# Optimization experiments

Hardware: AMD Instinct MI355X
Metric: run time of the kernel (lower is better)

The kernel has to match this reference:

```python
import math
import numpy as np
import jax, jax.numpy as jnp

# ---- e3nn-convention real Wigner 3j (small l, computed once in float64) ----

def _cg(j1, m1, j2, m2, j3, m3):
    if m3 != m1 + m2:
        return 0.0
    f = math.factorial
    vmin = max(-j1 + j2 + m3, -j1 + m1, 0)
    vmax = min(j2 + j3 + m1, j3 - j1 + j2, j3 + m3)
    c = math.sqrt((2 * j3 + 1) * f(j3 + j1 - j2) * f(j3 - j1 + j2) * f(j1 + j2 - j3)
                  * f(j3 + m3) * f(j3 - m3)
                  / (f(j1 + j2 + j3 + 1) * f(j1 - m1) * f(j1 + m1) * f(j2 - m2) * f(j2 + m2)))
    s = 0.0
    for v in range(vmin, vmax + 1):
        s += (-1.0) ** (v + j2 + m2) * f(j2 + j3 + m1 - v) * f(j1 - m1 + v) \
             / (f(v) * f(j3 - j1 + j2 - v) * f(j3 + m3 - v) * f(v + j1 - j2 - m3))
    return c * s


def _q(l):
    # real -> complex spherical-harmonic change of basis (e3nn convention)
    q = np.zeros((2 * l + 1, 2 * l + 1), dtype=np.complex128)
    for m in range(-l, 0):
        q[l + m, l + abs(m)] = 1.0 / math.sqrt(2)
        q[l + m, l - abs(m)] = -1j / math.sqrt(2)
    q[l, l] = 1.0
    for m in range(1, l + 1):
        q[l + m, l + abs(m)] = (-1) ** m / math.sqrt(2)
        q[l + m, l - abs(m)] = 1j * (-1) ** m / math.sqrt(2)
    return (-1j) ** l * q


def wigner_3j(l1, l2, l3):
    C = np.zeros((2 * l1 + 1, 2 * l2 + 1, 2 * l3 + 1))
    for m1 in range(-l1, l1 + 1):
        for m2 in range(-l2, l2 + 1):
            m3 = m1 + m2
            if -l3 <= m3 <= l3:
                C[m1 + l1, m2 + l2, m3 + l3] = _cg(l1, m1, l2, m2, l3, m3)
    Cr = np.einsum('ia,kb,mc,ikm->abc', _q(l1), _q(l2), np.conj(_q(l3)), C.astype(np.complex128))
    assert np.abs(Cr.imag).max() < 1e-8
    Cr = Cr.real
    return Cr / np.linalg.norm(Cr)  # unit Frobenius norm (e3nn wigner_3j)

W3J_101 = wigner_3j(1, 0, 1)  # (3,1,3)
W3J_121 = wigner_3j(1, 2, 1)  # (3,5,3)
W3J_221 = wigner_3j(2, 2, 1)  # (5,5,3)
W3J_321 = wigner_3j(3, 2, 1)  # (7,5,3)
W3J_110 = wigner_3j(1, 1, 0)
W3J_112 = wigner_3j(1, 1, 2)
# CartesianTensor('ij=ji') change of basis: symmetric 3x3 -> irreps 1x0e+1x2e, orthonormal rows
COB = np.concatenate([W3J_110[:, :, 0][None], math.sqrt(5.0) * np.moveaxis(W3J_112, 2, 0)], axis=0)  # (6,3,3)
# e3nn FullyConnectedTensorProduct path norm: irrep_normalization='component' (alpha=dim_out=3),
# path_normalization='element' (4 paths to same output, each mul1*mul2=2 elements -> x=8)
ALPHA = math.sqrt(3.0 / 8.0)
IDX = np.array([0, 4, 8, 1, 5, 6])  # xx,yy,zz,xy,yz,zx picks from flattened 3x3 jacobian

BS = 1_000_000


def setup_inputs():
    key = jax.random.key(0)
    node_feature = jax.random.normal(key, (BS, 64), dtype=jnp.float32)
    constant_w = jnp.ones((8,), dtype=jnp.float32)
    return {"node_feature": node_feature, "constant_w": constant_w}


def _piezo(node_feature, constant_w):
    bs = node_feature.shape[0]
    dt = node_feature.dtype
    # input irrep layout: 2x0e[0:2] 2x0o[2:4] 2x1e[4:10] 2x1o[10:16] 2x2e[16:26] 2x2o[26:36] 2x3e[36:50] 2x3o[50:64]
    x1o = node_feature[:, 10:16].reshape(bs, 2, 3)
    x2o = node_feature[:, 26:36].reshape(bs, 2, 5)
    x3o = node_feature[:, 50:64].reshape(bs, 2, 7)
    w = constant_w
    # D is bilinear in (node_feature, stress) and stress is linear in outer_S, so the three
    # autograd.grad calls in the original module exactly extract the (b,3,3,3) jacobian
    # dD/d(outer_S). Compute it analytically in one fused pass.
    # K[b,k,a] = dD[b,k]/dstress[b,a], stress irreps 1x0e(+)1x2e
    k0 = ALPHA * jnp.einsum('u,bui,ijk->bkj', w[0:2], x1o, jnp.asarray(W3J_101, dt))  # (b,3,1) from 0e
    k1 = ALPHA * jnp.einsum('u,bui,ijk->bkj', w[2:4], x1o, jnp.asarray(W3J_121, dt))  # (b,3,5) from 2e
    k2 = ALPHA * jnp.einsum('u,bui,ijk->bkj', w[4:6], x2o, jnp.asarray(W3J_221, dt))
    k3 = ALPHA * jnp.einsum('u,bui,ijk->bkj', w[6:8], x3o, jnp.asarray(W3J_321, dt))
    K = jnp.concatenate([k0, k1 + k2 + k3], axis=-1)  # (b,3,6)
    # chain rule through from_cartesian: stress[b,a] = sum_pq COB[a,p,q] * outer_S[b,p,q]
    J = jnp.einsum('bka,apq->bkpq', K, jnp.asarray(COB, dt)).reshape(bs, 3, 9)
    return J[:, :, IDX]  # (b, 3, 6)


def reference(node_feature, constant_w):
    return _piezo(node_feature, constant_w)
```

## Files before the change

### kernel.cpp

```cpp
#include <hip/hip_runtime.h>
#include <cmath>
#include <complex>
#include <algorithm>

#define TILE 256

struct PiezoConsts {
  float M1[3][3][6];
  float M2[3][3][6];
  float M3[5][3][6];
  float M4[7][3][6];
};

typedef std::complex<double> cd;

static double factd(int n) {
  static const double f[11] = {1,1,2,6,24,120,720,5040,40320,362880,3628800};
  return f[n];
}

static double cg_(int j1,int m1,int j2,int m2,int j3,int m3) {
  if (m3 != m1 + m2) return 0.0;
  int vmin = std::max(std::max(-j1 + j2 + m3, -j1 + m1), 0);
  int vmax = std::min(std::min(j2 + j3 + m1, j3 - j1 + j2), j3 + m3);
  double c = std::sqrt((2*j3+1) * factd(j3+j1-j2) * factd(j3-j1+j2) * factd(j1+j2-j3)
                       * factd(j3+m3) * factd(j3-m3)
                       / (factd(j1+j2+j3+1) * factd(j1-m1) * factd(j1+m1)
                          * factd(j2-m2) * factd(j2+m2)));
  double s = 0.0;
  for (int v = vmin; v <= vmax; ++v) {
    double sgn = ((v + j2 + m2) & 1) ? -1.0 : 1.0;
    s += sgn * factd(j2+j3+m1-v) * factd(j1-m1+v)
         / (factd(v) * factd(j3-j1+j2-v) * factd(j3+m3-v) * factd(v+j1-j2-m3));
  }
  return c * s;
}

static void q_mat(int l, cd q[7][7]) {
  for (int a=0;a<7;a++) for (int b=0;b<7;b++) q[a][b] = cd(0,0);
  double s2 = 1.0/std::sqrt(2.0);
  for (int m=-l; m<0; ++m) {
    q[l+m][l-m] = cd(s2, 0);
    q[l+m][l+m] = cd(0, -s2);
  }
  q[l][l] = cd(1,0);
  for (int m=1; m<=l; ++m) {
    double sg = (m & 1) ? -1.0 : 1.0;
    q[l+m][l+m] = cd(sg*s2, 0);
    q[l+m][l-m] = cd(0, sg*s2);
  }
  cd ph(1,0); const cd mi(0,-1);
  for (int t=0;t<l;t++) ph *= mi;
  int n = 2*l+1;
  for (int a=0;a<n;a++) for (int b=0;b<n;b++) q[a][b] *= ph;
}

static void wigner3j_(int l1,int l2,int l3,double* out) {
  int n1=2*l1+1, n2=2*l2+1, n3=2*l3+1;
  double C[7][7][7] = {};
  for (int m1=-l1;m1<=l1;m1++) for (int m2=-l2;m2<=l2;m2++) {
    int m3 = m1+m2;
    if (m3 >= -l3 && m3 <= l3)
      C[m1+l1][m2+l2][m3+l3] = cg_(l1,m1,l2,m2,l3,m3);
  }
  cd q1[7][7], q2[7][7], q3[7][7];
  q_mat(l1,q1); q_mat(l2,q2); q_mat(l3,q3);
  double nrm = 0.0;
  for (int a=0;a<n1;a++) for (int b=0;b<n2;b++) for (int c=0;c<n3;c++) {
    cd s(0,0);
    for (int i=0;i<n1;i++) for (int k=0;k<n2;k++) for (int m=0;m<n3;m++) {
      double Cv = C[i][k][m];
      if (Cv != 0.0) s += q1[i][a]*q2[k][b]*std::conj(q3[m][c])*Cv;
    }
    out[(a*n2+b)*n3+c] = s.real();
    nrm += s.real()*s.real();
  }
  nrm = std::sqrt(nrm);
  for (int t=0;t<n1*n2*n3;t++) out[t] /= nrm;
}

static void build_consts(PiezoConsts& K) {
  double W101[3*1*3], W121[3*5*3], W221[5*5*3], W321[7*5*3], W110[3*3*1], W112[3*3*5];
  wigner3j_(1,0,1,W101);
  wigner3j_(1,2,1,W121);
  wigner3j_(2,2,1,W221);
  wigner3j_(3,2,1,W321);
  wigner3j_(1,1,0,W110);
  wigner3j_(1,1,2,W112);
  double COBm[6][3][3];
  const double s5 = std::sqrt(5.0);
  for (int p=0;p<3;p++) for (int q=0;q<3;q++) {
    COBm[0][p][q] = W110[(p*3+q)*1+0];
    for (int j=0;j<5;j++) COBm[1+j][p][q] = s5 * W112[(p*3+q)*5+j];
  }
  const int IDXv[6] = {0,4,8,1,5,6};
  double T[6][6];
  for (int a=0;a<6;a++) for (int c=0;c<6;c++)
    T[a][c] = COBm[a][IDXv[c]/3][IDXv[c]%3];
  const double ALPHA = std::sqrt(3.0/8.0);
  for (int i=0;i<3;i++) for (int k=0;k<3;k++) for (int c=0;c<6;c++) {
    K.M1[i][k][c] = (float)(ALPHA * W101[(i*1+0)*3+k] * T[0][c]);
    double m2 = 0;
    for (int j=0;j<5;j++) m2 += W121[(i*5+j)*3+k] * T[1+j][c];
    K.M2[i][k][c] = (float)(ALPHA * m2);
  }
  for (int i=0;i<5;i++) for (int k=0;k<3;k++) for (int c=0;c<6;c++) {
    double m = 0;
    for (int j=0;j<5;j++) m += W221[(i*5+j)*3+k] * T[1+j][c];
    K.M3[i][k][c] = (float)(ALPHA * m);
  }
  for (int i=0;i<7;i++) for (int k=0;k<3;k++) for (int c=0;c<6;c++) {
    double m = 0;
    for (int j=0;j<5;j++) m += W321[(i*5+j)*3+k] * T[1+j][c];
    K.M4[i][k][c] = (float)(ALPHA * m);
  }
}

__global__ __launch_bounds__(TILE, 6) void piezo_kernel(
    const float* __restrict__ nf, const float* __restrict__ w8,
    float* __restrict__ out, int n, PiezoConsts C)
{
  __shared__ float lds[TILE * 19];
  const int tid = threadIdx.x;
  const int rowBase = blockIdx.x * TILE;
  const int row = rowBase + tid;
  const bool active = row < n;

  float4 A, B, Cc, D, E, F, G, H, I;
  if (active) {
    const float4* src = (const float4*)(nf + (size_t)row * 64);
    A  = src[2];
    B  = src[3];
    Cc = src[6];
    D  = src[7];
    E  = src[8];
    F  = src[12];
    G  = src[13];
    H  = src[14];
    I  = src[15];
  }

  float acc[3][6];
  #pragma unroll
  for (int k=0;k<3;k++)
    #pragma unroll
    for (int c=0;c<6;c++) acc[k][c] = 0.0f;

  if (active) {
    const float w0=w8[0], w1=w8[1], w2=w8[2], w3=w8[3];
    const float w4=w8[4], w5=w8[5], w6=w8[6], w7=w8[7];
    const float u1a[3] = {A.z, A.w, B.x};
    const float u1b[3] = {B.y, B.z, B.w};
    const float u2a[5] = {Cc.z, Cc.w, D.x, D.y, D.z};
    const float u2b[5] = {D.w, E.x, E.y, E.z, E.w};
    const float u3a[7] = {F.z, F.w, G.x, G.y, G.z, G.w, H.x};
    const float u3b[7] = {H.y, H.z, H.w, I.x, I.y, I.z, I.w};
    float y1[3], y2[3], y3[5], y4[7];
    #pragma unroll
    for (int i=0;i<3;i++) { y1[i]=w0*u1a[i]+w1*u1b[i]; y2[i]=w2*u1a[i]+w3*u1b[i]; }
    #pragma unroll
    for (int i=0;i<5;i++) { y3[i]=w4*u2a[i]+w5*u2b[i]; }
    #pragma unroll
    for (int i=0;i<7;i++) { y4[i]=w6*u3a[i]+w7*u3b[i]; }
    #pragma unroll
    for (int k=0;k<3;k++) {
      #pragma unroll
      for (int c=0;c<6;c++) {
        float a = 0.0f;
        #pragma unroll
        for (int i=0;i<3;i++) a += y1[i]*C.M1[i][k][c] + y2[i]*C.M2[i][k][c];
        #pragma unroll
        for (int i=0;i<5;i++) a += y3[i]*C.M3[i][k][c];
        #pragma unroll
        for (int i=0;i<7;i++) a += y4[i]*C.M4[i][k][c];
        acc[k][c] = a;
      }
    }
    float* p = &lds[tid * 19];
    #pragma unroll
    for (int k=0;k<3;k++)
      #pragma unroll
      for (int c=0;c<6;c++) p[k*6+c] = acc[k][c];
  }
  __syncthreads();

  const int nRows = (n - rowBase < TILE) ? (n - rowBase) : TILE;
  float* dst = out + (size_t)rowBase * 18;
  const int nOut = nRows * 18;
  for (int f = tid; f < nOut; f += TILE) {
    dst[f] = lds[(f / 18) * 19 + (f % 18)];
  }
}

extern "C" void kernel_launch(void* const* d_in, const int* in_sizes, int n_in,
                              void* d_out, int out_size, void* d_ws, size_t ws_size,
                              hipStream_t stream) {
  const float* nf = (const float*)d_in[0];
  const float* w  = (const float*)d_in[1];
  float* out = (float*)d_out;
  const int n = in_sizes[0] / 64;

  PiezoConsts C;
  build_consts(C);

  const int grid = (n + TILE - 1) / TILE;
  piezo_kernel<<<dim3(grid), dim3(TILE), 0, stream>>>(nf, w, out, n, C);
}
```

Measured before the change: 363.5 us.

## Process two rows per thread with a merged 18x18 matrix and direct stores

Merges the four per-irrep constant matrices into a single 18x18 matrix. Each thread now handles two rows, so every uniform constant load feeds two FMAs, which suits packed float2 math. The LDS staging, the barrier and the coalesced store loop are removed in favour of direct float2 stores per row. In exchange the grid is halved, register pressure rises (launch bounds lowered to 3 blocks), and the output writes become strided per thread rather than coalesced.

```diff
diff --git a/kernel.cpp b/kernel.cpp
--- a/kernel.cpp
+++ b/kernel.cpp
@@ -6,10 +6,7 @@
 #define TILE 256
 
 struct PiezoConsts {
-  float M1[3][3][6];
-  float M2[3][3][6];
-  float M3[5][3][6];
-  float M4[7][3][6];
+  float G[18][18];
 };
 
 typedef std::complex<double> cd;
@@ -99,96 +96,88 @@
     T[a][c] = COBm[a][IDXv[c]/3][IDXv[c]%3];
   const double ALPHA = std::sqrt(3.0/8.0);
   for (int i=0;i<3;i++) for (int k=0;k<3;k++) for (int c=0;c<6;c++) {
-    K.M1[i][k][c] = (float)(ALPHA * W101[(i*1+0)*3+k] * T[0][c]);
+    int o = k*6+c;
+    K.G[0+i][o] = (float)(ALPHA * W101[(i*1+0)*3+k] * T[0][c]);
     double m2 = 0;
     for (int j=0;j<5;j++) m2 += W121[(i*5+j)*3+k] * T[1+j][c];
-    K.M2[i][k][c] = (float)(ALPHA * m2);
+    K.G[3+i][o] = (float)(ALPHA * m2);
   }
   for (int i=0;i<5;i++) for (int k=0;k<3;k++) for (int c=0;c<6;c++) {
     double m = 0;
     for (int j=0;j<5;j++) m += W221[(i*5+j)*3+k] * T[1+j][c];
-    K.M3[i][k][c] = (float)(ALPHA * m);
+    K.G[6+i][k*6+c] = (float)(ALPHA * m);
   }
   for (int i=0;i<7;i++) for (int k=0;k<3;k++) for (int c=0;c<6;c++) {
     double m = 0;
     for (int j=0;j<5;j++) m += W321[(i*5+j)*3+k] * T[1+j][c];
-    K.M4[i][k][c] = (float)(ALPHA * m);
+    K.G[11+i][k*6+c] = (float)(ALPHA * m);
   }
 }
 
-__global__ __launch_bounds__(TILE, 6) void piezo_kernel(
+__global__ __launch_bounds__(TILE, 3) void piezo_kernel(
     const float* __restrict__ nf, const float* __restrict__ w8,
     float* __restrict__ out, int n, PiezoConsts C)
 {
-  __shared__ float lds[TILE * 19];
   const int tid = threadIdx.x;
-  const int rowBase = blockIdx.x * TILE;
-  const int row = rowBase + tid;
-  const bool active = row < n;
+  const long long base = (long long)blockIdx.x * (2 * TILE);
+  const long long r0 = base + tid;
+  const long long r1 = r0 + TILE;
+  const bool a0 = r0 < n, a1 = r1 < n;
+  const size_t s0 = (size_t)(a0 ? r0 : 0) * 64;
+  const size_t s1 = (size_t)(a1 ? r1 : 0) * 64;
 
-  float4 A, B, Cc, D, E, F, G, H, I;
-  if (active) {
-    const float4* src = (const float4*)(nf + (size_t)row * 64);
-    A  = src[2];
-    B  = src[3];
-    Cc = src[6];
-    D  = src[7];
-    E  = src[8];
-    F  = src[12];
-    G  = src[13];
-    H  = src[14];
-    I  = src[15];
+  float u0[36], u1[36];
+  {
+    const float4* p0 = (const float4*)(nf + s0);
+    const float4* p1 = (const float4*)(nf + s1);
+    float4* d0 = (float4*)u0;
+    float4* d1 = (float4*)u1;
+    d0[0] = p0[2];  d0[1] = p0[3];
+    d0[2] = p0[6];  d0[3] = p0[7];  d0[4] = p0[8];
+    d0[5] = p0[12]; d0[6] = p0[13]; d0[7] = p0[14]; d0[8] = p0[15];
+    d1[0] = p1[2];  d1[1] = p1[3];
+    d1[2] = p1[6];  d1[3] = p1[7];  d1[4] = p1[8];
+    d1[5] = p1[12]; d1[6] = p1[13]; d1[7] = p1[14]; d1[8] = p1[15];
   }
 
-  float acc[3][6];
+  const float w0=w8[0], w1=w8[1], w2=w8[2], w3=w8[3];
+  const float w4=w8[4], w5=w8[5], w6=w8[6], w7=w8[7];
+
+  float2 y[18];
   #pragma unroll
-  for (int k=0;k<3;k++)
+  for (int i=0;i<3;i++) {
+    y[i]   = make_float2(fmaf(w0,u0[2+i], w1*u0[5+i]),  fmaf(w0,u1[2+i], w1*u1[5+i]));
+    y[3+i] = make_float2(fmaf(w2,u0[2+i], w3*u0[5+i]),  fmaf(w2,u1[2+i], w3*u1[5+i]));
+  }
+  #pragma unroll
+  for (int i=0;i<5;i++)
+    y[6+i] = make_float2(fmaf(w4,u0[10+i], w5*u0[15+i]), fmaf(w4,u1[10+i], w5*u1[15+i]));
+  #pragma unroll
+  for (int i=0;i<7;i++)
+    y[11+i] = make_float2(fmaf(w6,u0[22+i], w7*u0[29+i]), fmaf(w6,u1[22+i], w7*u1[29+i]));
+
+  float2 acc[18];
+  #pragma unroll
+  for (int o=0;o<18;o++) acc[o] = make_float2(0.0f, 0.0f);
+  #pragma unroll
+  for (int t=0;t<18;t++) {
     #pragma unroll
-    for (int c=0;c<6;c++) acc[k][c] = 0.0f;
+    for (int o=0;o<18;o++) {
+      const float m = C.G[t][o];
+      acc[o].x = fmaf(y[t].x, m, acc[o].x);
+      acc[o].y = fmaf(y[t].y, m, acc[o].y);
+    }
+  }
 
-  if (active) {
-    const float w0=w8[0], w1=w8[1], w2=w8[2], w3=w8[3];
-    const float w4=w8[4], w5=w8[5], w6=w8[6], w7=w8[7];
-    const float u1a[3] = {A.z, A.w, B.x};
-    const float u1b[3] = {B.y, B.z, B.w};
-    const float u2a[5] = {Cc.z, Cc.w, D.x, D.y, D.z};
-    const float u2b[5] = {D.w, E.x, E.y, E.z, E.w};
-    const float u3a[7] = {F.z, F.w, G.x, G.y, G.z, G.w, H.x};
-    const float u3b[7] = {H.y, H.z, H.w, I.x, I.y, I.z, I.w};
-    float y1[3], y2[3], y3[5], y4[7];
+  if (a0) {
+    float2* d = (float2*)(out + (size_t)r0 * 18);
     #pragma unroll
-    for (int i=0;i<3;i++) { y1[i]=w0*u1a[i]+w1*u1b[i]; y2[i]=w2*u1a[i]+w3*u1b[i]; }
+    for (int j=0;j<9;j++) d[j] = make_float2(acc[2*j].x, acc[2*j+1].x);
+  }
+  if (a1) {
+    float2* d = (float2*)(out + (size_t)r1 * 18);
     #pragma unroll
-    for (int i=0;i<5;i++) { y3[i]=w4*u2a[i]+w5*u2b[i]; }
-    #pragma unroll
-    for (int i=0;i<7;i++) { y4[i]=w6*u3a[i]+w7*u3b[i]; }
-    #pragma unroll
-    for (int k=0;k<3;k++) {
-      #pragma unroll
-      for (int c=0;c<6;c++) {
-        float a = 0.0f;
-        #pragma unroll
-        for (int i=0;i<3;i++) a += y1[i]*C.M1[i][k][c] + y2[i]*C.M2[i][k][c];
-        #pragma unroll
-        for (int i=0;i<5;i++) a += y3[i]*C.M3[i][k][c];
-        #pragma unroll
-        for (int i=0;i<7;i++) a += y4[i]*C.M4[i][k][c];
-        acc[k][c] = a;
-      }
-    }
-    float* p = &lds[tid * 19];
-    #pragma unroll
-    for (int k=0;k<3;k++)
-      #pragma unroll
-      for (int c=0;c<6;c++) p[k*6+c] = acc[k][c];
-  }
-  __syncthreads();
-
-  const int nRows = (n - rowBase < TILE) ? (n - rowBase) : TILE;
-  float* dst = out + (size_t)rowBase * 18;
-  const int nOut = nRows * 18;
-  for (int f = tid; f < nOut; f += TILE) {
-    dst[f] = lds[(f / 18) * 19 + (f % 18)];
+    for (int j=0;j<9;j++) d[j] = make_float2(acc[2*j].y, acc[2*j+1].y);
   }
 }
 
@@ -203,6 +192,6 @@
   PiezoConsts C;
   build_consts(C);
 
-  const int grid = (n + TILE - 1) / TILE;
+  const int grid = (n + 2*TILE - 1) / (2*TILE);
   piezo_kernel<<<dim3(grid), dim3(TILE), 0, stream>>>(nf, w, out, n, C);
 }
```

Measured after the change: 372.7 us. 1.03x slower.
